# Kernel tuning notes

Hardware: AMD Instinct MI355X
Metric: run time of the kernel (lower is better)

The kernel has to match this reference:

```python
import jax, jax.numpy as jnp
import numpy as np

PRE_NMS_TOPK = 6000
POST_NMS_TOPK = 1000
NMS_THRESH = 0.7
MIN_SIZE = 16.0
N = 1_000_000
H, W = 800, 1333


def setup_inputs() -> dict:
    key = jax.random.key(0)
    ki, kx, ky, kw, kh, kd, kl = jax.random.split(key, 7)
    image = jax.random.normal(ki, (1, H, W, 3), jnp.float32)
    # realistic anchors: centers uniform over image, sizes in [8, 228)
    cx = jax.random.uniform(kx, (N,), jnp.float32) * W
    cy = jax.random.uniform(ky, (N,), jnp.float32) * H
    aw = jax.random.uniform(kw, (N,), jnp.float32) * 220.0 + 8.0
    ah = jax.random.uniform(kh, (N,), jnp.float32) * 220.0 + 8.0
    anchors = jnp.stack([cx - 0.5 * aw, cy - 0.5 * ah, cx + 0.5 * aw, cy + 0.5 * ah], axis=1)
    bbox_deltas = jax.random.normal(kd, (N, 4), jnp.float32) * 0.1
    logits = jax.random.normal(kl, (N, 1), jnp.float32)
    return {"image": image, "anchors": anchors, "bbox_deltas": bbox_deltas, "logits": logits}


def _iou_matrix(boxes):
    # boxes: [K,4] as (x1,y1,x2,y2); IoU is symmetric in axis labeling,
    # matching tf.image.non_max_suppression's overlap math.
    x1, y1, x2, y2 = boxes[:, 0], boxes[:, 1], boxes[:, 2], boxes[:, 3]
    area = (x2 - x1) * (y2 - y1)
    ix1 = jnp.maximum(x1[:, None], x1[None, :])
    iy1 = jnp.maximum(y1[:, None], y1[None, :])
    ix2 = jnp.minimum(x2[:, None], x2[None, :])
    iy2 = jnp.minimum(y2[:, None], y2[None, :])
    inter = jnp.maximum(ix2 - ix1, 0.0) * jnp.maximum(iy2 - iy1, 0.0)
    union = area[:, None] + area[None, :] - inter
    return jnp.where(union > 0.0, inter / union, 0.0)


def _sequential_nms(iou, valid, thresh):
    # iou: [K,K]; boxes are already sorted by descending score.
    K = iou.shape[0]
    idx = jnp.arange(K)

    def step(keep, inp):
        i, row = inp
        ki = keep[i]
        suppress = ki & (row > thresh) & (idx > i)
        return keep & ~suppress, ki

    _, kept = jax.lax.scan(step, valid, (idx, iou))
    return kept  # [K] bool, in sorted order


def reference(image, anchors, bbox_deltas, logits):
    height = jnp.float32(image.shape[1])
    width = jnp.float32(image.shape[2])

    # --- box decode ---
    wa = anchors[:, 2] - anchors[:, 0]
    ha = anchors[:, 3] - anchors[:, 1]
    xa = anchors[:, 0] + 0.5 * wa
    ya = anchors[:, 1] + 0.5 * ha
    x = bbox_deltas[:, 0] * wa + xa
    y = bbox_deltas[:, 1] * ha + ya
    w = jnp.exp(bbox_deltas[:, 2]) * wa
    h = jnp.exp(bbox_deltas[:, 3]) * ha
    x1 = jnp.clip(x - 0.5 * w, 0.0, width - 1.0)
    y1 = jnp.clip(y - 0.5 * h, 0.0, height - 1.0)
    x2 = jnp.clip(x + 0.5 * w, 0.0, width - 1.0)
    y2 = jnp.clip(y + 0.5 * h, 0.0, height - 1.0)
    proposals = jnp.stack([x1, y1, x2, y2], axis=1)  # [N,4]

    # --- min-size filter (mask instead of dynamic gather) ---
    valid = ((x2 - x1) >= MIN_SIZE) & ((y2 - y1) >= MIN_SIZE)
    scores = jnp.where(valid, jax.nn.sigmoid(logits[:, 0]), -jnp.inf)

    # --- pre-NMS top-k ---
    top_scores, top_idx = jax.lax.top_k(scores, PRE_NMS_TOPK)
    top_boxes = proposals[top_idx]              # [K,4]
    top_valid = top_scores > -jnp.inf

    # --- NMS ---
    iou = _iou_matrix(top_boxes)
    kept = _sequential_nms(iou, top_valid, NMS_THRESH)

    # --- pack kept boxes (in score order) into fixed [POST,4], zero-padded ---
    rank = jnp.cumsum(kept.astype(jnp.int32)) - 1
    slot = jnp.where(kept, rank, POST_NMS_TOPK)  # invalid -> dropped
    out = jnp.zeros((POST_NMS_TOPK, 4), top_boxes.dtype)
    out = out.at[slot].set(top_boxes, mode="drop")
    return out
```

## Files before the change

kernel.cpp:

```cpp
#include <hip/hip_runtime.h>
#include <stdint.h>
#include <math.h>

#define N_ANCH   1000000
#define N4       (N_ANCH / 4)
#define NBLK4    ((N4 + 1023) / 1024)
#define NBLK256  ((N4 + 255) / 256)
#define PRE_K    6000
#define POST_K   1000
#define WORDS    94
#define ROWS     6016
#define W_IMG    1333.0f
#define H_IMG    800.0f

#define NS       7168
#define RBLK     112

#define OLDK     16

#define OFF_KEYS   0x000000u
#define OFF_HIST1  0x400000u
#define OFF_HIST2  0x404000u
#define OFF_CTRL   0x410000u
#define OFF_CAND   0x410100u
#define OFF_BOXES  0x41F000u
#define OFF_VALID  0x437000u
#define OFF_MASK   0x440000u

__device__ __forceinline__ float ref_exp(float v) {
  return (float)exp((double)v);
}

__device__ __forceinline__ void decode_box(float ax, float ay, float az, float aw,
                                           float dx, float dy, float dz, float dw,
                                           float& x1, float& y1, float& x2, float& y2,
                                           bool& valid) {
  float wa = __fsub_rn(az, ax);
  float ha = __fsub_rn(aw, ay);
  float xa = __fadd_rn(ax, __fmul_rn(0.5f, wa));
  float ya = __fadd_rn(ay, __fmul_rn(0.5f, ha));
  float x  = __fadd_rn(__fmul_rn(dx, wa), xa);
  float y  = __fadd_rn(__fmul_rn(dy, ha), ya);
  float w  = __fmul_rn(ref_exp(dz), wa);
  float h  = __fmul_rn(ref_exp(dw), ha);
  float hw = __fmul_rn(0.5f, w);
  float hh = __fmul_rn(0.5f, h);
  x1 = fminf(fmaxf(__fsub_rn(x, hw), 0.0f), W_IMG - 1.0f);
  y1 = fminf(fmaxf(__fsub_rn(y, hh), 0.0f), H_IMG - 1.0f);
  x2 = fminf(fmaxf(__fadd_rn(x, hw), 0.0f), W_IMG - 1.0f);
  y2 = fminf(fmaxf(__fadd_rn(y, hh), 0.0f), H_IMG - 1.0f);
  valid = (__fsub_rn(x2, x1) >= 16.0f) && (__fsub_rn(y2, y1) >= 16.0f);
}

__device__ __forceinline__ uint32_t wave_iscan(uint32_t x, int lane) {
  #pragma unroll
  for (int off = 1; off < 64; off <<= 1) {
    uint32_t u = __shfl_up(x, off, 64);
    if (lane >= off) x += u;
  }
  return x;
}

__device__ __forceinline__ uint64_t bcast64(uint64_t v, int lane) {
  uint32_t lo = (uint32_t)__builtin_amdgcn_readlane((int)(uint32_t)v, lane);
  uint32_t hi = (uint32_t)__builtin_amdgcn_readlane((int)(uint32_t)(v >> 32), lane);
  return ((uint64_t)hi << 32) | lo;
}

__device__ __forceinline__ uint64_t shflxor64(uint64_t v, int m) {
  uint32_t lo = (uint32_t)__shfl_xor((int)(uint32_t)v, m, 64);
  uint32_t hi = (uint32_t)__shfl_xor((int)(uint32_t)(v >> 32), m, 64);
  return ((uint64_t)hi << 32) | lo;
}

__global__ void __launch_bounds__(256) k_decode(const float4* __restrict__ anchors,
                                                const float4* __restrict__ deltas,
                                                const float*  __restrict__ logits,
                                                uint32_t* __restrict__ keys) {
  int i = blockIdx.x * 256 + threadIdx.x;
  if (i >= N_ANCH) return;
  float4 a = anchors[i];
  float4 d = deltas[i];
  float wa = a.z - a.x, ha = a.w - a.y;
  float xa = a.x + 0.5f * wa, ya = a.y + 0.5f * ha;
  float x = d.x * wa + xa, y = d.y * ha + ya;
  float w = __expf(d.z) * wa, h = __expf(d.w) * ha;
  float fx1 = fminf(fmaxf(x - 0.5f * w, 0.0f), W_IMG - 1.0f);
  float fx2 = fminf(fmaxf(x + 0.5f * w, 0.0f), W_IMG - 1.0f);
  float fy1 = fminf(fmaxf(y - 0.5f * h, 0.0f), H_IMG - 1.0f);
  float fy2 = fminf(fmaxf(y + 0.5f * h, 0.0f), H_IMG - 1.0f);
  float X = fx2 - fx1, Y = fy2 - fy1;
  bool valid = (X >= 16.0f) && (Y >= 16.0f);
  if (fabsf(X - 16.0f) < 0.02f || fabsf(Y - 16.0f) < 0.02f) {
    float ex1, ey1, ex2, ey2; bool vv;
    decode_box(a.x, a.y, a.z, a.w, d.x, d.y, d.z, d.w, ex1, ey1, ex2, ey2, vv);
    valid = vv;
  }
  uint32_t u = __float_as_uint(logits[i]);
  uint32_t o = (u & 0x80000000u) ? ~u : (u | 0x80000000u);
  keys[i] = valid ? ~o : 0xFFFFFFFFu;
}

__global__ void __launch_bounds__(1024) k_histA(const uint4* __restrict__ keys4,
                                                uint32_t* __restrict__ hist1) {
  __shared__ uint32_t lh[4096];
  int tid = threadIdx.x, lane = tid & 63;
  for (int b = tid; b < 4096; b += 1024) lh[b] = 0u;
  __syncthreads();
  int i4 = blockIdx.x * 1024 + tid;
  uint32_t invc = 0;
  if (i4 < N4) {
    uint4 kk = keys4[i4];
    uint32_t ks[4] = { kk.x, kk.y, kk.z, kk.w };
    #pragma unroll
    for (int e = 0; e < 4; e++) {
      if (ks[e] != 0xFFFFFFFFu) atomicAdd(&lh[ks[e] >> 20], 1u);
      else invc++;
    }
  }
  #pragma unroll
  for (int off = 32; off > 0; off >>= 1) invc += __shfl_down(invc, off, 64);
  if (lane == 0 && invc) atomicAdd(&lh[4095], invc);
  __syncthreads();
  for (int b = tid; b < 4096; b += 1024) {
    uint32_t cv = lh[b];
    if (cv) atomicAdd(&hist1[b], cv);
  }
}

__global__ void __launch_bounds__(1024) k_cut1(const uint32_t* __restrict__ hist1,
                                               uint32_t* __restrict__ ctrl) {
  __shared__ uint32_t part[1024];
  int t = threadIdx.x;
  uint4 s4 = ((const uint4*)hist1)[t];
  uint32_t tot = s4.x + s4.y + s4.z + s4.w;
  part[t] = tot;
  __syncthreads();
  uint32_t inc = tot;
  for (int off = 1; off < 1024; off <<= 1) {
    uint32_t u = (t >= off) ? part[t - off] : 0u;
    __syncthreads();
    inc += u;
    part[t] = inc;
    __syncthreads();
  }
  uint32_t ex = inc - tot;
  if (ex < PRE_K && inc >= PRE_K) {
    uint32_t run = ex;
    uint32_t binv[4] = { s4.x, s4.y, s4.z, s4.w };
    for (int b = 0; b < 4; b++) {
      if (run + binv[b] >= PRE_K) { ctrl[2] = 4 * t + b; ctrl[3] = run; break; }
      run += binv[b];
    }
  }
  if (t == 1023 && inc < PRE_K) { ctrl[2] = 4095u; ctrl[3] = inc; }
}

__global__ void __launch_bounds__(256) k_hist2(const uint4* __restrict__ keys4,
                                               const uint32_t* __restrict__ ctrl,
                                               uint32_t* __restrict__ hist2) {
  __shared__ uint32_t lh[256];
  int tid = threadIdx.x;
  lh[tid] = 0u;
  __syncthreads();
  uint32_t c = ctrl[2];
  int i4 = blockIdx.x * 256 + tid;
  if (i4 < N4) {
    uint4 kk = keys4[i4];
    uint32_t ks[4] = { kk.x, kk.y, kk.z, kk.w };
    #pragma unroll
    for (int e = 0; e < 4; e++)
      if ((ks[e] >> 20) == c) atomicAdd(&lh[(ks[e] >> 12) & 0xFFu], 1u);
  }
  __syncthreads();
  uint32_t v = lh[tid];
  if (v) atomicAdd(&hist2[tid], v);
}

__global__ void __launch_bounds__(64) k_cut2(const uint32_t* __restrict__ hist2,
                                             uint32_t* __restrict__ ctrl) {
  int lane = threadIdx.x;
  uint32_t c = ctrl[2], base = ctrl[3];
  const uint32_t* p = hist2 + 4 * lane;
  uint32_t b0 = p[0], b1 = p[1], b2 = p[2], b3 = p[3];
  uint32_t tot = b0 + b1 + b2 + b3;
  uint32_t inc = wave_iscan(tot, lane);
  uint32_t ex = inc - tot;
  bool found = false;
  if (base + ex < PRE_K && base + inc >= PRE_K) {
    uint32_t run = base + ex;
    uint32_t binv[4] = { b0, b1, b2, b3 };
    for (int b = 0; b < 4; b++) {
      if (run + binv[b] >= PRE_K) { ctrl[1] = (c << 8) | (uint32_t)(4 * lane + b); found = true; break; }
      run += binv[b];
    }
  }
  uint64_t fb = __ballot(found);
  if (lane == 0 && fb == 0ull) ctrl[1] = 0xFFFFFu;
}

__global__ void __launch_bounds__(256) k_compact(const uint4* __restrict__ keys4,
                                                 const float* __restrict__ logits,
                                                 uint32_t* ctrl,
                                                 uint64_t* __restrict__ cand) {
  __shared__ uint32_t wcnt[4];
  __shared__ uint32_t bbase_s;
  int tid = threadIdx.x, lane = tid & 63, wv = tid >> 6;
  uint32_t T = ctrl[1];
  int i4 = blockIdx.x * 256 + tid;
  uint4 kk = make_uint4(~0u, ~0u, ~0u, ~0u);
  if (i4 < N4) kk = keys4[i4];
  uint32_t ks[4] = { kk.x, kk.y, kk.z, kk.w };
  bool pass[4]; uint64_t m[4];
  uint32_t tot = 0;
  #pragma unroll
  for (int e = 0; e < 4; e++) {
    pass[e] = (i4 < N4) && ((ks[e] >> 12) <= T);
    m[e] = __ballot(pass[e]);
    tot += (uint32_t)__popcll((unsigned long long)m[e]);
  }
  if (lane == 0) wcnt[wv] = tot;
  __syncthreads();
  if (tid == 0) {
    uint32_t bt = wcnt[0] + wcnt[1] + wcnt[2] + wcnt[3];
    bbase_s = bt ? atomicAdd(&ctrl[0], bt) : 0u;
  }
  __syncthreads();
  uint32_t wb = bbase_s;
  for (int w2 = 0; w2 < wv; w2++) wb += wcnt[w2];
  uint64_t lmask = (1ull << lane) - 1ull;
  #pragma unroll
  for (int e = 0; e < 4; e++) {
    if (pass[e]) {
      int i = 4 * i4 + e;
      uint32_t skey;
      if (ks[e] == 0xFFFFFFFFu) {
        skey = 0xFF800000u;
      } else {
        double xd = (double)logits[i];
        float s = (float)(1.0 / (1.0 + exp(-xd)));
        skey = 0x7FFFFFFFu & ~__float_as_uint(s);
      }
      uint32_t p = wb + (uint32_t)__popcll((unsigned long long)(m[e] & lmask));
      if (p < NS) cand[p] = ((uint64_t)skey << 20) | (uint32_t)i;
    }
    wb += (uint32_t)__popcll((unsigned long long)m[e]);
  }
}

__global__ void __launch_bounds__(256) k_rank(
    const uint32_t* __restrict__ ctrl,
    const uint64_t* __restrict__ cand,
    const float4* __restrict__ anchors,
    const float4* __restrict__ deltas,
    float4* __restrict__ boxes,
    uint32_t* __restrict__ valid) {
  __shared__ uint32_t part[4][64];
  int tid = threadIdx.x;
  int wv = tid >> 6, lane = tid & 63;
  int i = blockIdx.x * 64 + lane;
  uint32_t M = ctrl[0]; if (M > NS) M = NS;
  uint64_t myk = (i < (int)M) ? cand[i] : ~0ull;
  uint32_t cnt = 0;
  const int QUART = NS / 4;
  int jbase = wv * QUART;
  for (int s = 0; s < QUART / 64; s++) {
    int j = jbase + s * 64 + lane;
    uint64_t c = (j < (int)M) ? cand[j] : ~0ull;
    #pragma unroll
    for (int s2 = 0; s2 < 64; s2++) {
      uint64_t kb = bcast64(c, s2);
      cnt += (kb < myk) ? 1u : 0u;
    }
  }
  part[wv][lane] = cnt;
  __syncthreads();
  if (wv != 0) return;
  uint32_t rank = part[0][lane] + part[1][lane] + part[2][lane] + part[3][lane];
  if (i < (int)M && rank < PRE_K) {
    uint32_t skey = (uint32_t)(myk >> 20);
    uint32_t idx  = (uint32_t)(myk & 0xFFFFFu);
    if (skey >= 0xFF800000u) {
      boxes[rank] = make_float4(0.f, 0.f, 0.f, 0.f);
      valid[rank] = 0u;
    } else {
      float4 a = anchors[idx];
      float4 d = deltas[idx];
      float x1, y1, x2, y2; bool vv;
      decode_box(a.x, a.y, a.z, a.w, d.x, d.y, d.z, d.w, x1, y1, x2, y2, vv);
      boxes[rank] = make_float4(x1, y1, x2, y2);
      valid[rank] = 1u;
    }
  }
  if ((i >= (int)M || i >= PRE_K) && i < ROWS) {
    boxes[i] = make_float4(0.f, 0.f, 0.f, 0.f);
    valid[i] = 0u;
  }
}

__global__ void __launch_bounds__(64) k_iou(const float4* __restrict__ boxes,
                                            uint64_t* __restrict__ mask) {
  int by = blockIdx.y, bx = blockIdx.x;
  if (bx < by) return;
  __shared__ float4 cb[64];
  int t = threadIdx.x;
  cb[t] = boxes[bx * 64 + t];
  __syncthreads();
  int i = by * 64 + t;
  float4 b = boxes[i];
  float ax1 = b.x, ay1 = b.y, ax2 = b.z, ay2 = b.w;
  float areaA = __fmul_rn(__fsub_rn(ax2, ax1), __fsub_rn(ay2, ay1));
  uint64_t bits = 0;
  for (int c = 0; c < 64; c++) {
    float4 o = cb[c];
    float areaB = __fmul_rn(__fsub_rn(o.z, o.x), __fsub_rn(o.w, o.y));
    float ix1 = fmaxf(ax1, o.x), iy1 = fmaxf(ay1, o.y);
    float ix2 = fminf(ax2, o.z), iy2 = fminf(ay2, o.w);
    float iw = fmaxf(__fsub_rn(ix2, ix1), 0.0f);
    float ih = fmaxf(__fsub_rn(iy2, iy1), 0.0f);
    float inter = __fmul_rn(iw, ih);
    float uni = __fsub_rn(__fadd_rn(areaA, areaB), inter);
    bool sup = (uni > 0.0f) && (__fdiv_rn(inter, uni) > 0.7f);
    bits |= ((uint64_t)sup) << c;
  }
  mask[(size_t)i * WORDS + bx] = bits;
}

__global__ void __launch_bounds__(64, 1) k_nms(const uint64_t* __restrict__ mask,
                                               const float4* __restrict__ boxes,
                                               const uint32_t* __restrict__ valid,
                                               float* __restrict__ out) {
  __shared__ uint32_t list[1088];
  int lane = threadIdx.x;
  uint64_t lmask = (1ull << lane) - 1ull;
  int cnt = 0;
  uint64_t colv = mask[(size_t)lane * WORDS + 0];
  uint32_t vf = valid[lane];
  uint64_t cur = 0;
  for (int g = 0; g < WORDS; g++) {
    int base = g * 64;
    bool haveNext = (g + 1 < WORDS);
    uint64_t newv = 0, colv_n = 0, oldv[OLDK];
    uint32_t vf_n = 0, om = 0;
    if (haveNext) {
      newv   = mask[(size_t)(base + lane) * WORDS + (g + 1)];
      colv_n = mask[(size_t)(base + 64 + lane) * WORDS + (g + 1)];
      vf_n   = valid[base + 64 + lane];
      #pragma unroll
      for (int k = 0; k < OLDK; k++) {
        int t = 64 * k + lane;
        uint32_t row = (t < cnt) ? list[t] : 0u;
        om |= (t < cnt) ? (1u << k) : 0u;
        oldv[k] = mask[(size_t)row * WORDS + (g + 1)];
      }
    }
    uint64_t vmask = __ballot(vf != 0u);
    uint64_t alive = vmask & ~cur;
    uint64_t kept = 0;
    #pragma unroll
    for (int r = 0; r < 64; r++) {
      uint64_t mr = bcast64(colv, r);
      uint64_t take = (alive >> r) & 1ull;
      kept |= take << r;
      alive &= ~(take ? mr : 0ull);
    }
    uint32_t below = (uint32_t)__popcll((unsigned long long)(kept & lmask));
    if ((kept >> lane) & 1ull) {
      uint32_t pos = (uint32_t)cnt + below;
      if (pos < 1088u) list[pos] = (uint32_t)(base + lane);
    }
    cnt += (int)__popcll((unsigned long long)kept);
    if (cnt >= POST_K || !haveNext) break;
    asm volatile("" : "+v"(newv),
                      "+v"(oldv[0]),  "+v"(oldv[1]),  "+v"(oldv[2]),  "+v"(oldv[3]),
                      "+v"(oldv[4]),  "+v"(oldv[5]),  "+v"(oldv[6]),  "+v"(oldv[7]),
                      "+v"(oldv[8]),  "+v"(oldv[9]),  "+v"(oldv[10]), "+v"(oldv[11]),
                      "+v"(oldv[12]), "+v"(oldv[13]), "+v"(oldv[14]), "+v"(oldv[15]));
    uint64_t acc = ((kept >> lane) & 1ull) ? newv : 0ull;
    #pragma unroll
    for (int k = 0; k < OLDK; k++)
      acc |= oldv[k] & (0ull - (uint64_t)((om >> k) & 1u));
    #pragma unroll
    for (int off = 1; off < 64; off <<= 1)
      acc |= shflxor64(acc, off);
    cur = bcast64(acc, 0);
    colv = colv_n; vf = vf_n;
  }
  __syncthreads();
  float4* outv = (float4*)out;
  for (int k = lane; k < POST_K; k += 64)
    outv[k] = (k < cnt) ? boxes[list[k]] : make_float4(0.f, 0.f, 0.f, 0.f);
}

extern "C" void kernel_launch(void* const* d_in, const int* in_sizes, int n_in,
                              void* d_out, int out_size, void* d_ws, size_t ws_size,
                              hipStream_t stream) {
  const float4* anchors = (const float4*)d_in[1];
  const float4* deltas  = (const float4*)d_in[2];
  const float*  logits  = (const float*)d_in[3];
  char* w = (char*)d_ws;
  uint32_t* keys  = (uint32_t*)(w + OFF_KEYS);
  uint32_t* hist1 = (uint32_t*)(w + OFF_HIST1);
  uint32_t* hist2 = (uint32_t*)(w + OFF_HIST2);
  uint32_t* ctrl  = (uint32_t*)(w + OFF_CTRL);
  uint64_t* cand  = (uint64_t*)(w + OFF_CAND);
  float4*   boxes = (float4*)(w + OFF_BOXES);
  uint32_t* valid = (uint32_t*)(w + OFF_VALID);
  uint64_t* mask  = (uint64_t*)(w + OFF_MASK);
  float*    out   = (float*)d_out;

  hipMemsetAsync(w + OFF_HIST1, 0, 0x4400, stream);
  hipMemsetAsync(w + OFF_CTRL, 0, 256, stream);

  k_decode<<<(N_ANCH + 255) / 256, 256, 0, stream>>>(anchors, deltas, logits, keys);
  k_histA<<<NBLK4, 1024, 0, stream>>>((const uint4*)keys, hist1);
  k_cut1<<<1, 1024, 0, stream>>>(hist1, ctrl);
  k_hist2<<<NBLK256, 256, 0, stream>>>((const uint4*)keys, ctrl, hist2);
  k_cut2<<<1, 64, 0, stream>>>(hist2, ctrl);
  k_compact<<<NBLK256, 256, 0, stream>>>((const uint4*)keys, logits, ctrl, cand);
  k_rank<<<RBLK, 256, 0, stream>>>(ctrl, cand, anchors, deltas, boxes, valid);
  k_iou<<<dim3(WORDS, WORDS), 64, 0, stream>>>(boxes, mask);
  k_nms<<<1, 64, 0, stream>>>(mask, boxes, valid, out);
}
```

Before: 238.4 us.

## Fuse decode with 16-bit global histogram and replace two-pass radix select

Decode and key generation now build a 65536-bin histogram of the top 16 key bits directly with global atomics, using a grid-stride loop over a fixed number of blocks. A single cut kernel scans this histogram to find the threshold bin, which replaces the previous 12-bit histogram, cut, 8-bit refinement histogram and second cut. This removes three launches and two re-reads of the key array. In exchange it adds contended global atomics, a larger memset aliased onto the mask buffer, and a coarser threshold that may let more candidates into compaction.

```diff
diff --git a/kernel.cpp b/kernel.cpp
--- a/kernel.cpp
+++ b/kernel.cpp
@@ -4,8 +4,8 @@
 
 #define N_ANCH   1000000
 #define N4       (N_ANCH / 4)
-#define NBLK4    ((N4 + 1023) / 1024)
 #define NBLK256  ((N4 + 255) / 256)
+#define SBLK     977
 #define PRE_K    6000
 #define POST_K   1000
 #define WORDS    94
@@ -19,13 +19,12 @@
 #define OLDK     16
 
 #define OFF_KEYS   0x000000u
-#define OFF_HIST1  0x400000u
-#define OFF_HIST2  0x404000u
 #define OFF_CTRL   0x410000u
 #define OFF_CAND   0x410100u
 #define OFF_BOXES  0x41F000u
 #define OFF_VALID  0x437000u
 #define OFF_MASK   0x440000u
+#define OFF_HIST   OFF_MASK
 
 __device__ __forceinline__ float ref_exp(float v) {
   return (float)exp((double)v);
@@ -52,15 +51,6 @@
   valid = (__fsub_rn(x2, x1) >= 16.0f) && (__fsub_rn(y2, y1) >= 16.0f);
 }
 
-__device__ __forceinline__ uint32_t wave_iscan(uint32_t x, int lane) {
-  #pragma unroll
-  for (int off = 1; off < 64; off <<= 1) {
-    uint32_t u = __shfl_up(x, off, 64);
-    if (lane >= off) x += u;
-  }
-  return x;
-}
-
 __device__ __forceinline__ uint64_t bcast64(uint64_t v, int lane) {
   uint32_t lo = (uint32_t)__builtin_amdgcn_readlane((int)(uint32_t)v, lane);
   uint32_t hi = (uint32_t)__builtin_amdgcn_readlane((int)(uint32_t)(v >> 32), lane);
@@ -73,67 +63,54 @@
   return ((uint64_t)hi << 32) | lo;
 }
 
-__global__ void __launch_bounds__(256) k_decode(const float4* __restrict__ anchors,
-                                                const float4* __restrict__ deltas,
-                                                const float*  __restrict__ logits,
-                                                uint32_t* __restrict__ keys) {
-  int i = blockIdx.x * 256 + threadIdx.x;
-  if (i >= N_ANCH) return;
-  float4 a = anchors[i];
-  float4 d = deltas[i];
-  float wa = a.z - a.x, ha = a.w - a.y;
-  float xa = a.x + 0.5f * wa, ya = a.y + 0.5f * ha;
-  float x = d.x * wa + xa, y = d.y * ha + ya;
-  float w = __expf(d.z) * wa, h = __expf(d.w) * ha;
-  float fx1 = fminf(fmaxf(x - 0.5f * w, 0.0f), W_IMG - 1.0f);
-  float fx2 = fminf(fmaxf(x + 0.5f * w, 0.0f), W_IMG - 1.0f);
-  float fy1 = fminf(fmaxf(y - 0.5f * h, 0.0f), H_IMG - 1.0f);
-  float fy2 = fminf(fmaxf(y + 0.5f * h, 0.0f), H_IMG - 1.0f);
-  float X = fx2 - fx1, Y = fy2 - fy1;
-  bool valid = (X >= 16.0f) && (Y >= 16.0f);
-  if (fabsf(X - 16.0f) < 0.02f || fabsf(Y - 16.0f) < 0.02f) {
-    float ex1, ey1, ex2, ey2; bool vv;
-    decode_box(a.x, a.y, a.z, a.w, d.x, d.y, d.z, d.w, ex1, ey1, ex2, ey2, vv);
-    valid = vv;
-  }
-  uint32_t u = __float_as_uint(logits[i]);
-  uint32_t o = (u & 0x80000000u) ? ~u : (u | 0x80000000u);
-  keys[i] = valid ? ~o : 0xFFFFFFFFu;
-}
-
-__global__ void __launch_bounds__(1024) k_histA(const uint4* __restrict__ keys4,
-                                                uint32_t* __restrict__ hist1) {
-  __shared__ uint32_t lh[4096];
+__global__ void __launch_bounds__(256) k_score(const float4* __restrict__ anchors,
+                                               const float4* __restrict__ deltas,
+                                               const float*  __restrict__ logits,
+                                               uint32_t* __restrict__ keys,
+                                               uint32_t* __restrict__ hist) {
   int tid = threadIdx.x, lane = tid & 63;
-  for (int b = tid; b < 4096; b += 1024) lh[b] = 0u;
-  __syncthreads();
-  int i4 = blockIdx.x * 1024 + tid;
-  uint32_t invc = 0;
-  if (i4 < N4) {
-    uint4 kk = keys4[i4];
-    uint32_t ks[4] = { kk.x, kk.y, kk.z, kk.w };
-    #pragma unroll
-    for (int e = 0; e < 4; e++) {
-      if (ks[e] != 0xFFFFFFFFu) atomicAdd(&lh[ks[e] >> 20], 1u);
-      else invc++;
-    }
-  }
-  #pragma unroll
-  for (int off = 32; off > 0; off >>= 1) invc += __shfl_down(invc, off, 64);
-  if (lane == 0 && invc) atomicAdd(&lh[4095], invc);
-  __syncthreads();
-  for (int b = tid; b < 4096; b += 1024) {
-    uint32_t cv = lh[b];
-    if (cv) atomicAdd(&hist1[b], cv);
-  }
-}
-
-__global__ void __launch_bounds__(1024) k_cut1(const uint32_t* __restrict__ hist1,
-                                               uint32_t* __restrict__ ctrl) {
+  for (int i = blockIdx.x * 256 + tid; i < N_ANCH; i += SBLK * 256) {
+    float4 a = anchors[i];
+    float4 d = deltas[i];
+    float wa = a.z - a.x, ha = a.w - a.y;
+    float xa = a.x + 0.5f * wa, ya = a.y + 0.5f * ha;
+    float x = d.x * wa + xa, y = d.y * ha + ya;
+    float w = __expf(d.z) * wa, h = __expf(d.w) * ha;
+    float fx1 = fminf(fmaxf(x - 0.5f * w, 0.0f), W_IMG - 1.0f);
+    float fx2 = fminf(fmaxf(x + 0.5f * w, 0.0f), W_IMG - 1.0f);
+    float fy1 = fminf(fmaxf(y - 0.5f * h, 0.0f), H_IMG - 1.0f);
+    float fy2 = fminf(fmaxf(y + 0.5f * h, 0.0f), H_IMG - 1.0f);
+    float X = fx2 - fx1, Y = fy2 - fy1;
+    bool valid = (X >= 16.0f) && (Y >= 16.0f);
+    if (fabsf(X - 16.0f) < 0.02f || fabsf(Y - 16.0f) < 0.02f) {
+      float ex1, ey1, ex2, ey2; bool vv;
+      decode_box(a.x, a.y, a.z, a.w, d.x, d.y, d.z, d.w, ex1, ey1, ex2, ey2, vv);
+      valid = vv;
+    }
+    uint32_t u = __float_as_uint(logits[i]);
+    uint32_t o = (u & 0x80000000u) ? ~u : (u | 0x80000000u);
+    uint32_t kd = valid ? ~o : 0xFFFFFFFFu;
+    keys[i] = kd;
+    uint64_t invb = __ballot(!valid);
+    if (valid) {
+      atomicAdd(&hist[kd >> 16], 1u);
+    } else if ((invb & ((1ull << lane) - 1ull)) == 0ull) {
+      atomicAdd(&hist[0xFFFFu], (uint32_t)__popcll((unsigned long long)invb));
+    }
+  }
+}
+
+__global__ void __launch_bounds__(1024) k_cut16(const uint32_t* __restrict__ hist,
+                                                uint32_t* __restrict__ ctrl) {
   __shared__ uint32_t part[1024];
   int t = threadIdx.x;
-  uint4 s4 = ((const uint4*)hist1)[t];
-  uint32_t tot = s4.x + s4.y + s4.z + s4.w;
+  const uint4* h4 = (const uint4*)hist;
+  uint32_t tot = 0;
+  #pragma unroll
+  for (int k = 0; k < 16; k++) {
+    uint4 q = h4[t * 16 + k];
+    tot += q.x + q.y + q.z + q.w;
+  }
   part[t] = tot;
   __syncthreads();
   uint32_t inc = tot;
@@ -147,56 +124,16 @@
   uint32_t ex = inc - tot;
   if (ex < PRE_K && inc >= PRE_K) {
     uint32_t run = ex;
-    uint32_t binv[4] = { s4.x, s4.y, s4.z, s4.w };
-    for (int b = 0; b < 4; b++) {
-      if (run + binv[b] >= PRE_K) { ctrl[2] = 4 * t + b; ctrl[3] = run; break; }
-      run += binv[b];
-    }
-  }
-  if (t == 1023 && inc < PRE_K) { ctrl[2] = 4095u; ctrl[3] = inc; }
-}
-
-__global__ void __launch_bounds__(256) k_hist2(const uint4* __restrict__ keys4,
-                                               const uint32_t* __restrict__ ctrl,
-                                               uint32_t* __restrict__ hist2) {
-  __shared__ uint32_t lh[256];
-  int tid = threadIdx.x;
-  lh[tid] = 0u;
-  __syncthreads();
-  uint32_t c = ctrl[2];
-  int i4 = blockIdx.x * 256 + tid;
-  if (i4 < N4) {
-    uint4 kk = keys4[i4];
-    uint32_t ks[4] = { kk.x, kk.y, kk.z, kk.w };
-    #pragma unroll
-    for (int e = 0; e < 4; e++)
-      if ((ks[e] >> 20) == c) atomicAdd(&lh[(ks[e] >> 12) & 0xFFu], 1u);
-  }
-  __syncthreads();
-  uint32_t v = lh[tid];
-  if (v) atomicAdd(&hist2[tid], v);
-}
-
-__global__ void __launch_bounds__(64) k_cut2(const uint32_t* __restrict__ hist2,
-                                             uint32_t* __restrict__ ctrl) {
-  int lane = threadIdx.x;
-  uint32_t c = ctrl[2], base = ctrl[3];
-  const uint32_t* p = hist2 + 4 * lane;
-  uint32_t b0 = p[0], b1 = p[1], b2 = p[2], b3 = p[3];
-  uint32_t tot = b0 + b1 + b2 + b3;
-  uint32_t inc = wave_iscan(tot, lane);
-  uint32_t ex = inc - tot;
-  bool found = false;
-  if (base + ex < PRE_K && base + inc >= PRE_K) {
-    uint32_t run = base + ex;
-    uint32_t binv[4] = { b0, b1, b2, b3 };
-    for (int b = 0; b < 4; b++) {
-      if (run + binv[b] >= PRE_K) { ctrl[1] = (c << 8) | (uint32_t)(4 * lane + b); found = true; break; }
-      run += binv[b];
-    }
-  }
-  uint64_t fb = __ballot(found);
-  if (lane == 0 && fb == 0ull) ctrl[1] = 0xFFFFFu;
+    bool done = false;
+    for (int k = 0; k < 16 && !done; k++) {
+      uint4 q = h4[t * 16 + k];
+      uint32_t b[4] = { q.x, q.y, q.z, q.w };
+      for (int e = 0; e < 4; e++) {
+        if (run + b[e] >= PRE_K) { ctrl[1] = (uint32_t)(64 * t + 4 * k + e); done = true; break; }
+        run += b[e];
+      }
+    }
+  }
 }
 
 __global__ void __launch_bounds__(256) k_compact(const uint4* __restrict__ keys4,
@@ -215,7 +152,7 @@
   uint32_t tot = 0;
   #pragma unroll
   for (int e = 0; e < 4; e++) {
-    pass[e] = (i4 < N4) && ((ks[e] >> 12) <= T);
+    pass[e] = (i4 < N4) && ((ks[e] >> 16) <= T);
     m[e] = __ballot(pass[e]);
     tot += (uint32_t)__popcll((unsigned long long)m[e]);
   }
@@ -400,8 +337,7 @@
   const float*  logits  = (const float*)d_in[3];
   char* w = (char*)d_ws;
   uint32_t* keys  = (uint32_t*)(w + OFF_KEYS);
-  uint32_t* hist1 = (uint32_t*)(w + OFF_HIST1);
-  uint32_t* hist2 = (uint32_t*)(w + OFF_HIST2);
+  uint32_t* hist  = (uint32_t*)(w + OFF_HIST);
   uint32_t* ctrl  = (uint32_t*)(w + OFF_CTRL);
   uint64_t* cand  = (uint64_t*)(w + OFF_CAND);
   float4*   boxes = (float4*)(w + OFF_BOXES);
@@ -409,14 +345,11 @@
   uint64_t* mask  = (uint64_t*)(w + OFF_MASK);
   float*    out   = (float*)d_out;
 
-  hipMemsetAsync(w + OFF_HIST1, 0, 0x4400, stream);
+  hipMemsetAsync(w + OFF_HIST, 0, 0x40000, stream);
   hipMemsetAsync(w + OFF_CTRL, 0, 256, stream);
 
-  k_decode<<<(N_ANCH + 255) / 256, 256, 0, stream>>>(anchors, deltas, logits, keys);
-  k_histA<<<NBLK4, 1024, 0, stream>>>((const uint4*)keys, hist1);
-  k_cut1<<<1, 1024, 0, stream>>>(hist1, ctrl);
-  k_hist2<<<NBLK256, 256, 0, stream>>>((const uint4*)keys, ctrl, hist2);
-  k_cut2<<<1, 64, 0, stream>>>(hist2, ctrl);
+  k_score<<<SBLK, 256, 0, stream>>>(anchors, deltas, logits, keys, hist);
+  k_cut16<<<1, 1024, 0, stream>>>(hist, ctrl);
   k_compact<<<NBLK256, 256, 0, stream>>>((const uint4*)keys, logits, ctrl, cand);
   k_rank<<<RBLK, 256, 0, stream>>>(ctrl, cand, anchors, deltas, boxes, valid);
   k_iou<<<dim3(WORDS, WORDS), 64, 0, stream>>>(boxes, mask);
```

Result: slower. 495.0 us (+107.6%).
